# Performance work log

Hardware: AMD Instinct MI355X
Metric: run time of the kernel (lower is better)

The kernel has to match this reference:

```python
import jax, jax.numpy as jnp
import numpy as np

HEADS = 4
HEAD_DIM = 64  # hidden_dim 256 / 4 heads
REG_W = 1e-05
EPS = 1e-08


def setup_inputs() -> dict:
    key = jax.random.key(0)
    ks = jax.random.split(key, 8)
    B, N, H, R = 4, 2048, 256, 8

    def xavier(k, shape):
        fan_in, fan_out = shape[-1], shape[-2]
        lim = jnp.sqrt(6.0 / (fan_in + fan_out))
        return jax.random.uniform(k, shape, jnp.float32, -lim, lim)

    return {
        "x": jax.random.normal(ks[0], (B, N, H), jnp.float32),
        "w_qkv_low": xavier(ks[1], (3 * R, H)),
        "b_qkv_low": jnp.zeros((3 * R,), jnp.float32),
        "w_qkv_high": xavier(ks[2], (3 * H, 3 * R)),
        "b_qkv_high": jnp.zeros((3 * H,), jnp.float32),
        "w_out_low": xavier(ks[3], (R, H)),
        "b_out_low": jnp.zeros((R,), jnp.float32),
        "w_out_high": xavier(ks[4], (H, R)),
        "b_out_high": jnp.zeros((H,), jnp.float32),
        "adj_u": xavier(ks[5], (HEADS, N, R)),
        "adj_v": xavier(ks[6], (HEADS, R, N)),
    }


def reference(x, w_qkv_low, b_qkv_low, w_qkv_high, b_qkv_high,
              w_out_low, b_out_low, w_out_high, b_out_high, adj_u, adj_v):
    B, N, H = x.shape
    # Low-rank factorized QKV projection
    qkv_low = x @ w_qkv_low.T + b_qkv_low            # [B, N, 3r]
    qkv = qkv_low @ w_qkv_high.T + b_qkv_high        # [B, N, 3H]
    q, k, v = jnp.split(qkv, 3, axis=-1)
    # [B, N, H] -> [B, heads, N, head_dim]
    def to_heads(t):
        return t.reshape(B, N, HEADS, HEAD_DIM).transpose(0, 2, 1, 3)
    q, k, v = to_heads(q), to_heads(k), to_heads(v)

    # Linearized attention with ELU+1 feature map (uses local copies of q,k)
    qf = jax.nn.elu(q) + 1.0
    kf = jax.nn.elu(k) + 1.0
    kv = jnp.einsum('bhnd,bhne->bhde', kf, v)        # [B, h, d, d]
    z = 1.0 / (kf.sum(-1) + EPS)                     # [B, h, N]
    out = jnp.einsum('bhnd,bhde,bhn->bhne', qf, kv, z)

    # Full softmax attention with low-rank adjacency bias (only its L1 mean is used)
    adj_bias = jnp.einsum('hnr,hrm->hnm', adj_u, adj_v)          # [h, N, N]
    scores = jnp.einsum('bhnd,bhmd->bhnm', q, k) / np.sqrt(HEAD_DIM)
    attn = jax.nn.softmax(scores + adj_bias, axis=-1)
    attn_reg_loss = REG_W * jnp.mean(jnp.abs(attn))

    # Merge heads and low-rank output projection
    out = out.transpose(0, 2, 1, 3).reshape(B, N, H)
    out = out @ w_out_low.T + b_out_low
    out = out @ w_out_high.T + b_out_high
    return out, attn_reg_loss
```

## Files before the change

kernel.cpp:

```cpp
#include <hip/hip_runtime.h>
#include <math.h>

#define B_     4
#define N_     2048
#define H_     256
#define ROWS   8192
#define EPS_   1e-8f
#define REGW   1e-5f
#define OUT_MAIN (ROWS*H_)

static __device__ __forceinline__ float elu1(float x) {
    return x > 0.f ? x + 1.f : __expf(x);
}

static __device__ __forceinline__ void stage_whT(
    const float* __restrict__ wsrc, float* __restrict__ dst, int t)
{
#pragma unroll
    for (int i = 0; i < 6; i++) {
        int g = t + i * 256;
        float4 v4 = *(const float4*)(wsrc + g * 4);
        int e = g * 4, j = e / 24, k = e - j * 24;
        dst[(k + 0) * 260 + j] = v4.x;
        dst[(k + 1) * 260 + j] = v4.y;
        dst[(k + 2) * 260 + j] = v4.z;
        dst[(k + 3) * 260 + j] = v4.w;
    }
}

__global__ __launch_bounds__(256) void ka_ql(
    const float* __restrict__ x, const float* __restrict__ w_low,
    const float* __restrict__ b_low, float* __restrict__ g_ql,
    float* __restrict__ out)
{
    __shared__ float bufA[24 * 260];
    const int t = threadIdx.x;
    const size_t rowbase = (size_t)blockIdx.x * 16;
    const int rb = t >> 4, c4 = t & 15;

    if (blockIdx.x == 0 && t == 0)
        out[OUT_MAIN] = REGW / (float)N_;

#pragma unroll
    for (int i = 0; i < 6; i++) {
        int g = t + i * 256;
        int j = g >> 6, k = (g & 63) * 4;
        *(float4*)&bufA[j * 260 + k] = *(const float4*)(w_low + g * 4);
    }
    float4 xr[4];
#pragma unroll
    for (int i = 0; i < 4; i++)
        xr[i] = *(const float4*)(x + (rowbase + rb) * H_ + i * 64 + c4 * 4);
    __syncthreads();

    float ql[24];
#pragma unroll
    for (int j = 0; j < 24; j++) {
        float s = 0.f;
#pragma unroll
        for (int i = 0; i < 4; i++) {
            float4 w4 = *(const float4*)&bufA[j * 260 + i * 64 + c4 * 4];
            s += xr[i].x * w4.x + xr[i].y * w4.y + xr[i].z * w4.z + xr[i].w * w4.w;
        }
        s += __shfl_xor(s, 1, 16);
        s += __shfl_xor(s, 2, 16);
        s += __shfl_xor(s, 4, 16);
        s += __shfl_xor(s, 8, 16);
        ql[j] = s + b_low[j];
    }
    float v1 = 0.f, v2 = 0.f;
#pragma unroll
    for (int j = 0; j < 16; j++) if (c4 == j) v1 = ql[j];
#pragma unroll
    for (int j = 0; j < 8; j++)  if (c4 == j) v2 = ql[16 + j];
    size_t row = rowbase + rb;
    g_ql[(size_t)c4 * ROWS + row] = v1;
    if (c4 < 8) g_ql[(size_t)(16 + c4) * ROWS + row] = v2;
}

__global__ __launch_bounds__(256) void k2_kvz(
    const float* __restrict__ g_ql, const float* __restrict__ w_high,
    const float* __restrict__ b_high, float* __restrict__ zg,
    float* __restrict__ kvp)
{
    __shared__ float wkT[24 * 64];
    __shared__ float wvT[24 * 64];
    __shared__ float qls[24 * 64];
    __shared__ float kfs[64 * 68];
    __shared__ float vss[64 * 68];

    const int blk = blockIdx.x, t = threadIdx.x;
    const int b = blk >> 7, h = (blk >> 5) & 3, ch = blk & 31;
    const int rowb = b * N_ + ch * 64;

#pragma unroll
    for (int i = 0; i < 2; i++) {
        int g = t + i * 256;
        if (g < 384) {
            float4 a4 = *(const float4*)(w_high + 6144 + h * 1536 + g * 4);
            float4 b4 = *(const float4*)(w_high + 12288 + h * 1536 + g * 4);
            int e = g * 4, d = e / 24, kk = e - d * 24;
            wkT[(kk + 0) * 64 + d] = a4.x;
            wkT[(kk + 1) * 64 + d] = a4.y;
            wkT[(kk + 2) * 64 + d] = a4.z;
            wkT[(kk + 3) * 64 + d] = a4.w;
            wvT[(kk + 0) * 64 + d] = b4.x;
            wvT[(kk + 1) * 64 + d] = b4.y;
            wvT[(kk + 2) * 64 + d] = b4.z;
            wvT[(kk + 3) * 64 + d] = b4.w;
        }
    }
#pragma unroll
    for (int i = 0; i < 2; i++) {
        int g = t + i * 256;
        if (g < 384) {
            int kk = g >> 4, r4 = g & 15;
            *(float4*)&qls[kk * 64 + r4 * 4] =
                *(const float4*)(g_ql + (size_t)kk * ROWS + rowb + r4 * 4);
        }
    }
    __syncthreads();

    const int gR = t >> 4, c4 = t & 15;

    {
        float4 bh4 = *(const float4*)(b_high + 256 + h * 64 + c4 * 4);
        float4 acc[4];
#pragma unroll
        for (int rr = 0; rr < 4; rr++) acc[rr] = bh4;
#pragma unroll
        for (int kk = 0; kk < 24; kk++) {
            float4 w4 = *(const float4*)&wkT[kk * 64 + c4 * 4];
            float4 qa = *(const float4*)&qls[kk * 64 + gR * 4];
            acc[0].x += qa.x * w4.x; acc[0].y += qa.x * w4.y; acc[0].z += qa.x * w4.z; acc[0].w += qa.x * w4.w;
            acc[1].x += qa.y * w4.x; acc[1].y += qa.y * w4.y; acc[1].z += qa.y * w4.z; acc[1].w += qa.y * w4.w;
            acc[2].x += qa.z * w4.x; acc[2].y += qa.z * w4.y; acc[2].z += qa.z * w4.z; acc[2].w += qa.z * w4.w;
            acc[3].x += qa.w * w4.x; acc[3].y += qa.w * w4.y; acc[3].z += qa.w * w4.z; acc[3].w += qa.w * w4.w;
        }
#pragma unroll
        for (int rr = 0; rr < 4; rr++) {
            float4 a = acc[rr];
            a.x = elu1(a.x); a.y = elu1(a.y); a.z = elu1(a.z); a.w = elu1(a.w);
            *(float4*)&kfs[(gR * 4 + rr) * 68 + c4 * 4] = a;
            float s = a.x + a.y + a.z + a.w;
            s += __shfl_xor(s, 1, 16);
            s += __shfl_xor(s, 2, 16);
            s += __shfl_xor(s, 4, 16);
            s += __shfl_xor(s, 8, 16);
            if (c4 == 0)
                zg[(size_t)(rowb + gR * 4 + rr) * 4 + h] = 1.f / (s + EPS_);
        }
    }
    {
        float4 bh4 = *(const float4*)(b_high + 512 + h * 64 + c4 * 4);
        float4 acc[4];
#pragma unroll
        for (int rr = 0; rr < 4; rr++) acc[rr] = bh4;
#pragma unroll
        for (int kk = 0; kk < 24; kk++) {
            float4 w4 = *(const float4*)&wvT[kk * 64 + c4 * 4];
            float4 qa = *(const float4*)&qls[kk * 64 + gR * 4];
            acc[0].x += qa.x * w4.x; acc[0].y += qa.x * w4.y; acc[0].z += qa.x * w4.z; acc[0].w += qa.x * w4.w;
            acc[1].x += qa.y * w4.x; acc[1].y += qa.y * w4.y; acc[1].z += qa.y * w4.z; acc[1].w += qa.y * w4.w;
            acc[2].x += qa.z * w4.x; acc[2].y += qa.z * w4.y; acc[2].z += qa.z * w4.z; acc[2].w += qa.z * w4.w;
            acc[3].x += qa.w * w4.x; acc[3].y += qa.w * w4.y; acc[3].z += qa.w * w4.z; acc[3].w += qa.w * w4.w;
        }
#pragma unroll
        for (int rr = 0; rr < 4; rr++)
            *(float4*)&vss[(gR * 4 + rr) * 68 + c4 * 4] = acc[rr];
    }
    __syncthreads();

    const int d0 = (t >> 4) * 4, e0 = (t & 15) * 4;
    float4 a0 = {0,0,0,0}, a1 = {0,0,0,0}, a2 = {0,0,0,0}, a3 = {0,0,0,0};
#pragma unroll 4
    for (int i = 0; i < 64; i++) {
        float4 kk4 = *(const float4*)&kfs[i * 68 + d0];
        float4 v4 = *(const float4*)&vss[i * 68 + e0];
        a0.x += kk4.x * v4.x; a0.y += kk4.x * v4.y; a0.z += kk4.x * v4.z; a0.w += kk4.x * v4.w;
        a1.x += kk4.y * v4.x; a1.y += kk4.y * v4.y; a1.z += kk4.y * v4.z; a1.w += kk4.y * v4.w;
        a2.x += kk4.z * v4.x; a2.y += kk4.z * v4.y; a2.z += kk4.z * v4.z; a2.w += kk4.z * v4.w;
        a3.x += kk4.w * v4.x; a3.y += kk4.w * v4.y; a3.z += kk4.w * v4.z; a3.w += kk4.w * v4.w;
    }
    float* outp = kvp + (size_t)blk * 4096;
    *(float4*)(outp + (d0 + 0) * 64 + e0) = a0;
    *(float4*)(outp + (d0 + 1) * 64 + e0) = a1;
    *(float4*)(outp + (d0 + 2) * 64 + e0) = a2;
    *(float4*)(outp + (d0 + 3) * 64 + e0) = a3;
}

__global__ __launch_bounds__(256) void k2b_reduce(
    const float* __restrict__ kvp, float* __restrict__ kvg)
{
    const int blk = blockIdx.x, t = threadIdx.x;
    const int bh = blk >> 2, q = blk & 3;
    const int f4i = q * 256 + t;
    const float* src = kvp + (size_t)(bh * 32) * 4096 + f4i * 4;
    float4 s = {0.f, 0.f, 0.f, 0.f};
#pragma unroll
    for (int cc = 0; cc < 32; cc++) {
        float4 p = *(const float4*)(src + (size_t)cc * 4096);
        s.x += p.x; s.y += p.y; s.z += p.z; s.w += p.w;
    }
    *(float4*)(kvg + (size_t)bh * 4096 + f4i * 4) = s;
}

__global__ __launch_bounds__(256) void k4_out(
    const float* __restrict__ g_ql, const float* __restrict__ w_high,
    const float* __restrict__ b_high, const float* __restrict__ zg,
    const float* __restrict__ kvg,
    const float* __restrict__ w_out_low, const float* __restrict__ b_out_low,
    const float* __restrict__ w_out_high, const float* __restrict__ b_out_high,
    float* __restrict__ out)
{
    __shared__ float bufW[24 * 260];
    __shared__ float qfs[4 * 1092];
    __shared__ float qlT[24 * 16];
    __shared__ float lows[16 * 8];
    __shared__ float zs[64];
    float* lin = bufW;

    const int t = threadIdx.x, blk = blockIdx.x;
    const int rowbase = blk * 16;
    const int b = blk >> 7;
    const float* kvb = kvg + (size_t)b * 4 * 4096;

    stage_whT(w_high, bufW, t);
    {
        int k = t >> 4, r = t & 15;
        qlT[t] = g_ql[(size_t)k * ROWS + rowbase + r];
        if (t < 128) {
            int idx2 = 256 + t;
            int k2 = idx2 >> 4, r2 = idx2 & 15;
            qlT[idx2] = g_ql[(size_t)k2 * ROWS + rowbase + r2];
        }
    }
    if (t < 64) zs[t] = zg[(size_t)rowbase * 4 + t];
    __syncthreads();

    const int wv = t >> 6, c = t & 63;
    const int h = c >> 4, e4 = c & 15;

    {
        float4 bh4 = *(const float4*)(b_high + c * 4);
        float4 a0 = bh4, a1 = bh4, a2 = bh4, a3 = bh4;
#pragma unroll
        for (int k = 0; k < 24; k++) {
            float4 w4 = *(const float4*)&bufW[k * 260 + c * 4];
            float4 q4 = *(const float4*)&qlT[k * 16 + wv * 4];
            a0.x += q4.x * w4.x; a0.y += q4.x * w4.y; a0.z += q4.x * w4.z; a0.w += q4.x * w4.w;
            a1.x += q4.y * w4.x; a1.y += q4.y * w4.y; a1.z += q4.y * w4.z; a1.w += q4.y * w4.w;
            a2.x += q4.z * w4.x; a2.y += q4.z * w4.y; a2.z += q4.z * w4.z; a2.w += q4.z * w4.w;
            a3.x += q4.w * w4.x; a3.y += q4.w * w4.y; a3.z += q4.w * w4.z; a3.w += q4.w * w4.w;
        }
        float4 aa[4] = {a0, a1, a2, a3};
#pragma unroll
        for (int rr = 0; rr < 4; rr++) {
            float4 a = aa[rr];
            a.x = elu1(a.x); a.y = elu1(a.y); a.z = elu1(a.z); a.w = elu1(a.w);
            *(float4*)&qfs[h * 1092 + (wv * 4 + rr) * 68 + e4 * 4] = a;
        }
    }
    __syncthreads();

    {
        float4 acc[4] = {{0,0,0,0},{0,0,0,0},{0,0,0,0},{0,0,0,0}};
        const float* kvh = kvb + h * 4096 + e4 * 4;
        const float* qrow = &qfs[h * 1092 + (wv * 4) * 68];
#pragma unroll
        for (int d4 = 0; d4 < 16; d4++) {
            float4 k0 = *(const float4*)(kvh + (d4 * 4 + 0) * 64);
            float4 k1 = *(const float4*)(kvh + (d4 * 4 + 1) * 64);
            float4 k2 = *(const float4*)(kvh + (d4 * 4 + 2) * 64);
            float4 k3 = *(const float4*)(kvh + (d4 * 4 + 3) * 64);
#pragma unroll
            for (int rr = 0; rr < 4; rr++) {
                float4 qa = *(const float4*)(qrow + rr * 68 + d4 * 4);
                acc[rr].x += qa.x * k0.x + qa.y * k1.x + qa.z * k2.x + qa.w * k3.x;
                acc[rr].y += qa.x * k0.y + qa.y * k1.y + qa.z * k2.y + qa.w * k3.y;
                acc[rr].z += qa.x * k0.z + qa.y * k1.z + qa.z * k2.z + qa.w * k3.z;
                acc[rr].w += qa.x * k0.w + qa.y * k1.w + qa.z * k2.w + qa.w * k3.w;
            }
        }
#pragma unroll
        for (int rr = 0; rr < 4; rr++) {
            float zv = zs[(wv * 4 + rr) * 4 + h];
            *(float4*)&lin[(wv * 4 + rr) * 260 + c * 4] =
                make_float4(acc[rr].x * zv, acc[rr].y * zv,
                            acc[rr].z * zv, acc[rr].w * zv);
        }
    }
    __syncthreads();

    if (t < 128) {
        int rr = t >> 3, j = t & 7;
        float a = b_out_low[j];
        const float4* wj = (const float4*)(w_out_low + j * H_);
#pragma unroll
        for (int kq = 0; kq < 64; kq++) {
            float4 l4 = *(const float4*)&lin[rr * 260 + kq * 4];
            float4 w4 = wj[kq];
            a += l4.x * w4.x + l4.y * w4.y + l4.z * w4.z + l4.w * w4.w;
        }
        lows[rr * 8 + j] = a;
    }
    __syncthreads();

    {
        int rr = t >> 4, ig = t & 15;
        float l[8];
#pragma unroll
        for (int j = 0; j < 8; j++) l[j] = lows[rr * 8 + j];
        float* outp = out + (size_t)(rowbase + rr) * H_;
#pragma unroll
        for (int i16 = 0; i16 < 4; i16++) {
            int i = i16 * 64 + ig * 4;
            const float* wh = w_out_high + i * 8;
            float4 s;
            s.x = b_out_high[i + 0]; s.y = b_out_high[i + 1];
            s.z = b_out_high[i + 2]; s.w = b_out_high[i + 3];
#pragma unroll
            for (int j = 0; j < 8; j++) {
                s.x += l[j] * wh[j];
                s.y += l[j] * wh[8 + j];
                s.z += l[j] * wh[16 + j];
                s.w += l[j] * wh[24 + j];
            }
            *(float4*)(outp + i) = s;
        }
    }
}

extern "C" void kernel_launch(void* const* d_in, const int* in_sizes, int n_in,
                              void* d_out, int out_size, void* d_ws, size_t ws_size,
                              hipStream_t stream) {
    const float* x          = (const float*)d_in[0];
    const float* w_qkv_low  = (const float*)d_in[1];
    const float* b_qkv_low  = (const float*)d_in[2];
    const float* w_qkv_high = (const float*)d_in[3];
    const float* b_qkv_high = (const float*)d_in[4];
    const float* w_out_low  = (const float*)d_in[5];
    const float* b_out_low  = (const float*)d_in[6];
    const float* w_out_high = (const float*)d_in[7];
    const float* b_out_high = (const float*)d_in[8];
    char* wsb = (char*)d_ws;
    float* g_ql = (float*)(wsb);
    float* zg   = (float*)(wsb + ((size_t)0x100000));
    float* kvg  = (float*)(wsb + ((size_t)0x140000));
    float* kvp  = (float*)(wsb + ((size_t)0x200000));
    float* out = (float*)d_out;

    ka_ql<<<512, 256, 0, stream>>>(x, w_qkv_low, b_qkv_low, g_ql, out);
    k2_kvz<<<512, 256, 0, stream>>>(g_ql, w_qkv_high, b_qkv_high, zg, kvp);
    k2b_reduce<<<64, 256, 0, stream>>>(kvp, kvg);
    k4_out<<<512, 256, 0, stream>>>(g_ql, w_qkv_high, b_qkv_high, zg, kvg,
                                    w_out_low, b_out_low, w_out_high,
                                    b_out_high, out);
}
```

Baseline: 129.8 us.

## Fuse low-rank QKV projection into the KV/Z accumulation kernel

Merges the first low-rank projection kernel into the kv/z kernel. Each block now computes its 64 rows of the rank-24 projection into shared memory and reuses it directly, so the global round trip of g_ql and one launch are removed. Only head-0 blocks write g_ql for the later output kernel. In exchange, each of the four head blocks recomputes the same x projection, so reads of x and the projection work are repeated four times, and shared memory is aliased and grows per block.

New measurement: 152.9 us. 17.8% more time.

```diff
diff --git a/kernel.cpp b/kernel.cpp
--- a/kernel.cpp
+++ b/kernel.cpp
@@ -28,70 +28,79 @@
     }
 }
 
-__global__ __launch_bounds__(256) void ka_ql(
+__global__ __launch_bounds__(256) void k1_qkv(
     const float* __restrict__ x, const float* __restrict__ w_low,
-    const float* __restrict__ b_low, float* __restrict__ g_ql,
+    const float* __restrict__ b_low, const float* __restrict__ w_high,
+    const float* __restrict__ b_high, float* __restrict__ g_ql,
+    float* __restrict__ zg, float* __restrict__ kvp,
     float* __restrict__ out)
 {
-    __shared__ float bufA[24 * 260];
-    const int t = threadIdx.x;
-    const size_t rowbase = (size_t)blockIdx.x * 16;
-    const int rb = t >> 4, c4 = t & 15;
-
-    if (blockIdx.x == 0 && t == 0)
+    __shared__ float qls[24 * 64];
+    __shared__ float big[11776];
+    float* wlow = big;
+    float* wkT  = big;
+    float* wvT  = big + 1536;
+    float* kfs  = big + 3072;
+    float* vss  = big + 7424;
+
+    const int blk = blockIdx.x, t = threadIdx.x;
+    const int b = blk >> 7, h = (blk >> 5) & 3, ch = blk & 31;
+    const int rowb = b * N_ + ch * 64;
+
+    if (blk == 0 && t == 0)
         out[OUT_MAIN] = REGW / (float)N_;
 
 #pragma unroll
     for (int i = 0; i < 6; i++) {
         int g = t + i * 256;
         int j = g >> 6, k = (g & 63) * 4;
-        *(float4*)&bufA[j * 260 + k] = *(const float4*)(w_low + g * 4);
-    }
-    float4 xr[4];
-#pragma unroll
-    for (int i = 0; i < 4; i++)
-        xr[i] = *(const float4*)(x + (rowbase + rb) * H_ + i * 64 + c4 * 4);
-    __syncthreads();
-
-    float ql[24];
-#pragma unroll
-    for (int j = 0; j < 24; j++) {
-        float s = 0.f;
-#pragma unroll
-        for (int i = 0; i < 4; i++) {
-            float4 w4 = *(const float4*)&bufA[j * 260 + i * 64 + c4 * 4];
-            s += xr[i].x * w4.x + xr[i].y * w4.y + xr[i].z * w4.z + xr[i].w * w4.w;
-        }
-        s += __shfl_xor(s, 1, 16);
-        s += __shfl_xor(s, 2, 16);
-        s += __shfl_xor(s, 4, 16);
-        s += __shfl_xor(s, 8, 16);
-        ql[j] = s + b_low[j];
-    }
-    float v1 = 0.f, v2 = 0.f;
-#pragma unroll
-    for (int j = 0; j < 16; j++) if (c4 == j) v1 = ql[j];
-#pragma unroll
-    for (int j = 0; j < 8; j++)  if (c4 == j) v2 = ql[16 + j];
-    size_t row = rowbase + rb;
-    g_ql[(size_t)c4 * ROWS + row] = v1;
-    if (c4 < 8) g_ql[(size_t)(16 + c4) * ROWS + row] = v2;
-}
-
-__global__ __launch_bounds__(256) void k2_kvz(
-    const float* __restrict__ g_ql, const float* __restrict__ w_high,
-    const float* __restrict__ b_high, float* __restrict__ zg,
-    float* __restrict__ kvp)
-{
-    __shared__ float wkT[24 * 64];
-    __shared__ float wvT[24 * 64];
-    __shared__ float qls[24 * 64];
-    __shared__ float kfs[64 * 68];
-    __shared__ float vss[64 * 68];
-
-    const int blk = blockIdx.x, t = threadIdx.x;
-    const int b = blk >> 7, h = (blk >> 5) & 3, ch = blk & 31;
-    const int rowb = b * N_ + ch * 64;
+        *(float4*)&wlow[j * 260 + k] = *(const float4*)(w_low + g * 4);
+    }
+    __syncthreads();
+
+    const int rb = t >> 4, c4 = t & 15;
+    for (int cc = 0; cc < 4; cc++) {
+        const size_t row = (size_t)rowb + cc * 16 + rb;
+        float4 xr[4];
+#pragma unroll
+        for (int i = 0; i < 4; i++)
+            xr[i] = *(const float4*)(x + row * H_ + i * 64 + c4 * 4);
+        float ql[24];
+#pragma unroll
+        for (int j = 0; j < 24; j++) {
+            float s = 0.f;
+#pragma unroll
+            for (int i = 0; i < 4; i++) {
+                float4 w4 = *(const float4*)&wlow[j * 260 + i * 64 + c4 * 4];
+                s += xr[i].x * w4.x + xr[i].y * w4.y + xr[i].z * w4.z + xr[i].w * w4.w;
+            }
+            s += __shfl_xor(s, 1, 16);
+            s += __shfl_xor(s, 2, 16);
+            s += __shfl_xor(s, 4, 16);
+            s += __shfl_xor(s, 8, 16);
+            ql[j] = s + b_low[j];
+        }
+        float v1 = 0.f, v2 = 0.f;
+#pragma unroll
+        for (int j = 0; j < 16; j++) if (c4 == j) v1 = ql[j];
+#pragma unroll
+        for (int j = 0; j < 8; j++)  if (c4 == j) v2 = ql[16 + j];
+        qls[c4 * 64 + cc * 16 + rb] = v1;
+        if (c4 < 8) qls[(16 + c4) * 64 + cc * 16 + rb] = v2;
+    }
+    __syncthreads();
+
+    if (h == 0) {
+#pragma unroll
+        for (int i = 0; i < 2; i++) {
+            int g = t + i * 256;
+            if (g < 384) {
+                int kk = g >> 4, r4 = g & 15;
+                *(float4*)(g_ql + (size_t)kk * ROWS + rowb + r4 * 4) =
+                    *(const float4*)&qls[kk * 64 + r4 * 4];
+            }
+        }
+    }
 
 #pragma unroll
     for (int i = 0; i < 2; i++) {
@@ -110,18 +119,9 @@
             wvT[(kk + 3) * 64 + d] = b4.w;
         }
     }
-#pragma unroll
-    for (int i = 0; i < 2; i++) {
-        int g = t + i * 256;
-        if (g < 384) {
-            int kk = g >> 4, r4 = g & 15;
-            *(float4*)&qls[kk * 64 + r4 * 4] =
-                *(const float4*)(g_ql + (size_t)kk * ROWS + rowb + r4 * 4);
-        }
-    }
-    __syncthreads();
-
-    const int gR = t >> 4, c4 = t & 15;
+    __syncthreads();
+
+    const int gR = t >> 4;
 
     {
         float4 bh4 = *(const float4*)(b_high + 256 + h * 64 + c4 * 4);
@@ -350,8 +350,8 @@
     float* kvp  = (float*)(wsb + ((size_t)0x200000));
     float* out = (float*)d_out;
 
-    ka_ql<<<512, 256, 0, stream>>>(x, w_qkv_low, b_qkv_low, g_ql, out);
-    k2_kvz<<<512, 256, 0, stream>>>(g_ql, w_qkv_high, b_qkv_high, zg, kvp);
+    k1_qkv<<<512, 256, 0, stream>>>(x, w_qkv_low, b_qkv_low, w_qkv_high,
+                                    b_qkv_high, g_ql, zg, kvp, out);
     k2b_reduce<<<64, 256, 0, stream>>>(kvp, kvg);
     k4_out<<<512, 256, 0, stream>>>(g_ql, w_qkv_high, b_qkv_high, zg, kvg,
                                     w_out_low, b_out_low, w_out_high,
```
